# Performance work log

Hardware: AMD Instinct MI355X
Metric: run time of the kernel (lower is better)

The kernel has to match this reference:

```python
import jax, jax.numpy as jnp
import numpy as np

S, H, A = 16384, 1024, 1024


def setup_inputs() -> dict:
    key = jax.random.key(0)
    k1, k2, k3, k4, k5, k6 = jax.random.split(key, 6)
    enc_out = jax.random.normal(k1, (S, 1, H), dtype=jnp.float32)
    dec_h = jax.random.normal(k2, (1, H), dtype=jnp.float32)
    mask = jax.random.randint(k3, (S, 1), 0, 2) == 1  # bool [S,1]
    # learned params (torch Linear stores weight as [out, in]; y = x @ W.T)
    W2_dec = jax.random.normal(k4, (A, H), dtype=jnp.float32) * 0.02
    W1_enc = jax.random.normal(k5, (A, H), dtype=jnp.float32) * 0.02
    V = jax.random.normal(k6, (1, A), dtype=jnp.float32) * 0.02
    return {"enc_out": enc_out, "dec_h": dec_h, "mask": mask,
            "W2_dec": W2_dec, "W1_enc": W1_enc, "V": V}


def reference(enc_out, dec_h, mask, W2_dec, W1_enc, V):
    enc = jnp.squeeze(enc_out, axis=1)            # [S, H]
    d = dec_h @ W2_dec.T                          # [1, A]
    e = enc @ W1_enc.T                            # [S, A]
    u = jnp.tanh(d + e) @ V.T                     # [S, 1]
    u = jnp.where(mask, -jnp.inf, u)              # masked logits (returned, like in-place fill)
    a = jax.nn.softmax(u, axis=0)                 # softmax over seq dim
    out = jnp.sum(a * enc, axis=0)                # [H]
    return (out, u)
```

## Files before the change

kernel.cpp:

```cpp
#include <hip/hip_runtime.h>
#include <math.h>
#include <stdint.h>

#define S_DIM 16384
#define H_DIM 1024
#define A_DIM 1024

#define MASK_NEG (-3.0e38f)

typedef __attribute__((ext_vector_type(8))) _Float16 f16x8;
typedef __attribute__((ext_vector_type(4))) float f32x4;
typedef __attribute__((address_space(3))) uint32_t as3_u32;
typedef __attribute__((address_space(1))) uint32_t as1_u32;

__global__ __launch_bounds__(256) void prep_kernel(
        const float* __restrict__ enc, _Float16* __restrict__ enc_h,
        const float* __restrict__ W1, _Float16* __restrict__ W1_h,
        const float* __restrict__ dec_h, const float* __restrict__ W2,
        float* __restrict__ d, float* __restrict__ u_acc) {
    const int b = blockIdx.x;
    const int t = threadIdx.x;
    if (b < 8704) {
        const float* src = (b < 8192) ? enc : W1;
        _Float16* dst    = (b < 8192) ? enc_h : W1_h;
        const int i = ((b < 8192) ? b : (b - 8192)) * 256 + t;
        float4 v0 = ((const float4*)src)[2 * i];
        float4 v1 = ((const float4*)src)[2 * i + 1];
        union { _Float16 h[8]; uint4 u; } pk;
        pk.h[0] = (_Float16)v0.x; pk.h[1] = (_Float16)v0.y;
        pk.h[2] = (_Float16)v0.z; pk.h[3] = (_Float16)v0.w;
        pk.h[4] = (_Float16)v1.x; pk.h[5] = (_Float16)v1.y;
        pk.h[6] = (_Float16)v1.z; pk.h[7] = (_Float16)v1.w;
        ((uint4*)dst)[i] = pk.u;
        if (b < 64) u_acc[b * 256 + t] = 0.0f;
    } else {
        const int a = b - 8704;
        const float* row = W2 + (size_t)a * H_DIM;
        float s = 0.0f;
        for (int h = t; h < H_DIM; h += 256) s += dec_h[h] * row[h];
        #pragma unroll
        for (int off = 32; off; off >>= 1) s += __shfl_down(s, off, 64);
        __shared__ float wsum[4];
        if ((t & 63) == 0) wsum[t >> 6] = s;
        __syncthreads();
        if (t == 0) d[a] = wsum[0] + wsum[1] + wsum[2] + wsum[3];
    }
}

__global__ __launch_bounds__(512, 2) void fused_gemm_f16(
        const _Float16* __restrict__ Ag,
        const _Float16* __restrict__ Bg,
        const float* __restrict__ V,
        const float* __restrict__ d,
        float* __restrict__ u_acc) {
    __shared__ __align__(16) _Float16 AB[2][16384];

    const int tid  = threadIdx.x;
    const int wave = tid >> 6;
    const int lane = tid & 63;
    const int quad = lane >> 4;
    const int l16  = lane & 15;
    const int wm   = wave >> 2;
    const int wn   = wave & 3;
    const int s0   = blockIdx.x * 256;
    const int a0   = blockIdx.y * 256;

    const _Float16* gsrc = (wave < 4) ? Ag : Bg;
    const int rbase      = (wave < 4) ? s0 : a0;
    const int rowoff     = (wave & 3) * 64;
    const int lrow = lane >> 2;
    const int cg   = ((lane & 3) + (lrow >> 1)) & 3;

    const _Float16* grow[4];
    #pragma unroll
    for (int j = 0; j < 4; ++j)
        grow[j] = gsrc + (size_t)(rbase + rowoff + j * 16 + lrow) * H_DIM + cg * 8;
    _Float16* lbase0 = &AB[0][((wave < 4) ? 0 : 8192) + rowoff * 32];

    const int sw = ((quad - (l16 >> 1)) & 3) * 8;
    int aoff[8], boff[4];
    #pragma unroll
    for (int mi = 0; mi < 8; ++mi)
        aoff[mi] = (wm * 128 + mi * 16 + l16) * 32 + sw;
    #pragma unroll
    for (int ni = 0; ni < 4; ++ni)
        boff[ni] = 8192 + (wn * 64 + ni * 16 + l16) * 32 + sw;

    f32x4 acc[8][4];
    #pragma unroll
    for (int mi = 0; mi < 8; ++mi)
        #pragma unroll
        for (int ni = 0; ni < 4; ++ni)
            acc[mi][ni] = (f32x4){0.f, 0.f, 0.f, 0.f};

    #pragma unroll
    for (int j = 0; j < 4; ++j)
        __builtin_amdgcn_global_load_lds(
            (const as1_u32*)(const void*)(grow[j]),
            (as3_u32*)(void*)(lbase0 + j * 512), 16, 0, 0);
    __syncthreads();

    for (int kt = 0; kt < H_DIM / 32; kt += 2) {
        {
            #pragma unroll
            for (int j = 0; j < 4; ++j)
                __builtin_amdgcn_global_load_lds(
                    (const as1_u32*)(const void*)(grow[j] + (kt + 1) * 32),
                    (as3_u32*)(void*)(lbase0 + 16384 + j * 512), 16, 0, 0);
        }
        {
            f16x8 bf[4];
            #pragma unroll
            for (int ni = 0; ni < 4; ++ni) bf[ni] = *(const f16x8*)&AB[0][boff[ni]];
            #pragma unroll
            for (int mi = 0; mi < 8; ++mi) {
                f16x8 af = *(const f16x8*)&AB[0][aoff[mi]];
                #pragma unroll
                for (int ni = 0; ni < 4; ++ni)
                    acc[mi][ni] = __builtin_amdgcn_mfma_f32_16x16x32_f16(af, bf[ni], acc[mi][ni], 0, 0, 0);
            }
        }
        __syncthreads();

        if (kt + 2 < H_DIM / 32) {
            #pragma unroll
            for (int j = 0; j < 4; ++j)
                __builtin_amdgcn_global_load_lds(
                    (const as1_u32*)(const void*)(grow[j] + (kt + 2) * 32),
                    (as3_u32*)(void*)(lbase0 + j * 512), 16, 0, 0);
        }
        {
            f16x8 bf[4];
            #pragma unroll
            for (int ni = 0; ni < 4; ++ni) bf[ni] = *(const f16x8*)&AB[1][boff[ni]];
            #pragma unroll
            for (int mi = 0; mi < 8; ++mi) {
                f16x8 af = *(const f16x8*)&AB[1][aoff[mi]];
                #pragma unroll
                for (int ni = 0; ni < 4; ++ni)
                    acc[mi][ni] = __builtin_amdgcn_mfma_f32_16x16x32_f16(af, bf[ni], acc[mi][ni], 0, 0, 0);
            }
        }
        __syncthreads();
    }

    float* P = (float*)&AB[0][0];
    float vv[4], dd[4];
    #pragma unroll
    for (int ni = 0; ni < 4; ++ni) {
        int c = a0 + wn * 64 + ni * 16 + l16;
        vv[ni] = V[c];
        dd[ni] = d[c];
    }
    #pragma unroll
    for (int mi = 0; mi < 8; ++mi) {
        #pragma unroll
        for (int reg = 0; reg < 4; ++reg) {
            float s = 0.0f;
            #pragma unroll
            for (int ni = 0; ni < 4; ++ni)
                s += vv[ni] * tanhf(dd[ni] + acc[mi][ni][reg]);
            #pragma unroll
            for (int off = 1; off < 16; off <<= 1)
                s += __shfl_xor(s, off, 64);
            if (l16 == 0)
                P[(wm * 128 + mi * 16 + quad * 4 + reg) * 4 + wn] = s;
        }
    }
    __syncthreads();
    if (tid < 256)
        atomicAdd(u_acc + s0 + tid,
                  P[tid * 4 + 0] + P[tid * 4 + 1] + P[tid * 4 + 2] + P[tid * 4 + 3]);
}

__global__ __launch_bounds__(256) void fused_gemm(const float* __restrict__ enc,
                                                  const float* __restrict__ W1,
                                                  const float* __restrict__ V,
                                                  const float* __restrict__ d,
                                                  float* __restrict__ u_acc) {
    __shared__ __align__(16) float As[16][128 + 4];
    __shared__ __align__(16) float Bs[16][128 + 4];
    const int tid = threadIdx.x;
    const int tx = tid & 15, ty = tid >> 4;
    const int s0 = blockIdx.y * 128, a0 = blockIdx.x * 128;
    const int lr = tid >> 2, lc = tid & 3;
    float acc[8][8] = {};
    for (int kt = 0; kt < H_DIM / 16; ++kt) {
        const int k0 = kt * 16;
        float4 av0 = *(const float4*)(enc + (size_t)(s0 + lr)      * H_DIM + k0 + 4 * lc);
        float4 av1 = *(const float4*)(enc + (size_t)(s0 + lr + 64) * H_DIM + k0 + 4 * lc);
        float4 bv0 = *(const float4*)(W1  + (size_t)(a0 + lr)      * H_DIM + k0 + 4 * lc);
        float4 bv1 = *(const float4*)(W1  + (size_t)(a0 + lr + 64) * H_DIM + k0 + 4 * lc);
        __syncthreads();
        As[4*lc+0][lr] = av0.x; As[4*lc+1][lr] = av0.y; As[4*lc+2][lr] = av0.z; As[4*lc+3][lr] = av0.w;
        As[4*lc+0][lr+64] = av1.x; As[4*lc+1][lr+64] = av1.y; As[4*lc+2][lr+64] = av1.z; As[4*lc+3][lr+64] = av1.w;
        Bs[4*lc+0][lr] = bv0.x; Bs[4*lc+1][lr] = bv0.y; Bs[4*lc+2][lr] = bv0.z; Bs[4*lc+3][lr] = bv0.w;
        Bs[4*lc+0][lr+64] = bv1.x; Bs[4*lc+1][lr+64] = bv1.y; Bs[4*lc+2][lr+64] = bv1.z; Bs[4*lc+3][lr+64] = bv1.w;
        __syncthreads();
        #pragma unroll
        for (int k = 0; k < 16; ++k) {
            float4 A0 = *(const float4*)&As[k][8 * ty];
            float4 A1 = *(const float4*)&As[k][8 * ty + 4];
            float4 B0 = *(const float4*)&Bs[k][8 * tx];
            float4 B1 = *(const float4*)&Bs[k][8 * tx + 4];
            float ar[8] = {A0.x, A0.y, A0.z, A0.w, A1.x, A1.y, A1.z, A1.w};
            float br[8] = {B0.x, B0.y, B0.z, B0.w, B1.x, B1.y, B1.z, B1.w};
            #pragma unroll
            for (int i = 0; i < 8; ++i)
                #pragma unroll
                for (int j = 0; j < 8; ++j)
                    acc[i][j] = fmaf(ar[i], br[j], acc[i][j]);
        }
    }
    float vv[8], dd[8];
    #pragma unroll
    for (int j = 0; j < 8; ++j) { int c = a0 + 8 * tx + j; vv[j] = V[c]; dd[j] = d[c]; }
    float pu[8];
    #pragma unroll
    for (int i = 0; i < 8; ++i) {
        float s = 0.0f;
        #pragma unroll
        for (int j = 0; j < 8; ++j) s += vv[j] * tanhf(dd[j] + acc[i][j]);
        pu[i] = s;
    }
    __syncthreads();
    float* Pf = &As[0][0];
    #pragma unroll
    for (int i = 0; i < 8; ++i) Pf[(8 * ty + i) * 16 + tx] = pu[i];
    __syncthreads();
    if (tid < 128) {
        float s = 0.0f;
        #pragma unroll
        for (int j = 0; j < 16; ++j) s += Pf[tid * 16 + j];
        atomicAdd(u_acc + s0 + tid, s);
    }
}

__global__ __launch_bounds__(1024) void softmax_kernel(const float* __restrict__ u_acc,
                                                       const void* __restrict__ mask,
                                                       float* __restrict__ u_out,
                                                       float* __restrict__ p) {
    const int t = threadIdx.x;
    const unsigned char* mb = (const unsigned char*)mask;
    const int* mi = (const int*)mask;

    unsigned int orv = 0;
    for (int i = t; i < S_DIM; i += 1024)
        if (i & 3) orv |= mb[i];
    __shared__ int sflag;
    if (t == 0) sflag = 0;
    __syncthreads();
    if (orv) sflag = 1;
    __syncthreads();
    const int bytemask = sflag;

    float v[16];
    float lmax = -INFINITY;
    #pragma unroll
    for (int i = 0; i < 16; ++i) {
        int r = t + i * 1024;
        int m = bytemask ? (int)mb[r] : mi[r];
        float val = m ? MASK_NEG : u_acc[r];
        u_out[r] = val;
        v[i] = val;
        lmax = fmaxf(lmax, val);
    }

    __shared__ float red[16];
    __shared__ float sm, sdenom;
    #pragma unroll
    for (int off = 32; off; off >>= 1) lmax = fmaxf(lmax, __shfl_down(lmax, off, 64));
    int wid = t >> 6, lane = t & 63;
    if (lane == 0) red[wid] = lmax;
    __syncthreads();
    if (t == 0) {
        float m2 = -INFINITY;
        for (int i = 0; i < 16; ++i) m2 = fmaxf(m2, red[i]);
        sm = m2;
    }
    __syncthreads();
    const float m = sm;

    float lsum = 0.0f;
    #pragma unroll
    for (int i = 0; i < 16; ++i) {
        v[i] = expf(v[i] - m);
        lsum += v[i];
    }
    #pragma unroll
    for (int off = 32; off; off >>= 1) lsum += __shfl_down(lsum, off, 64);
    if (lane == 0) red[wid] = lsum;
    __syncthreads();
    if (t == 0) {
        float s2 = 0.0f;
        for (int i = 0; i < 16; ++i) s2 += red[i];
        sdenom = s2;
    }
    __syncthreads();
    const float inv = 1.0f / sdenom;
    #pragma unroll
    for (int i = 0; i < 16; ++i) p[t + i * 1024] = v[i] * inv;
}

__global__ __launch_bounds__(256) void wsum_part(const _Float16* __restrict__ enc_h,
                                                 const float* __restrict__ p,
                                                 float* __restrict__ part) {
    const int t = threadIdx.x;
    const int b = blockIdx.x;
    float4 acc = {0.f, 0.f, 0.f, 0.f};
    const int s0 = b * 32;
    for (int s = s0; s < s0 + 32; ++s) {
        float ps = p[s];
        union { _Float16 h[4]; uint2 u; } e;
        e.u = ((const uint2*)(enc_h + (size_t)s * H_DIM))[t];
        acc.x += ps * (float)e.h[0];
        acc.y += ps * (float)e.h[1];
        acc.z += ps * (float)e.h[2];
        acc.w += ps * (float)e.h[3];
    }
    ((float4*)(part + (size_t)b * 1024))[t] = acc;
}
__global__ __launch_bounds__(256) void wsum_reduce(const float* __restrict__ part,
                                                   float* __restrict__ out) {
    __shared__ float red[256];
    const int t = threadIdx.x;
    const int col = blockIdx.x * 16 + (t & 15);
    const int seg = t >> 4;
    float s = 0.0f;
    for (int b = seg * 32; b < seg * 32 + 32; ++b)
        s += part[(size_t)b * 1024 + col];
    red[t] = s;
    __syncthreads();
    if (t < 16) {
        float r = 0.0f;
        #pragma unroll
        for (int k = 0; k < 16; ++k) r += red[k * 16 + t];
        out[col] = r;
    }
}
__global__ __launch_bounds__(256) void weighted_sum(const float* __restrict__ enc,
                                                    const float* __restrict__ p,
                                                    float* __restrict__ out) {
    const int t = threadIdx.x;
    const int s0 = blockIdx.x * 32;
    const float4* encv = (const float4*)enc;
    float4 acc = {0.0f, 0.0f, 0.0f, 0.0f};
    for (int s = s0; s < s0 + 32; ++s) {
        float ps = p[s];
        float4 e = encv[(size_t)s * 256 + t];
        acc.x += ps * e.x; acc.y += ps * e.y; acc.z += ps * e.z; acc.w += ps * e.w;
    }
    atomicAdd(out + 4 * t + 0, acc.x);
    atomicAdd(out + 4 * t + 1, acc.y);
    atomicAdd(out + 4 * t + 2, acc.z);
    atomicAdd(out + 4 * t + 3, acc.w);
}
__global__ void zero_kernel(float* __restrict__ u_acc, float* __restrict__ out) {
    int i = blockIdx.x * 256 + threadIdx.x;
    if (i < S_DIM) u_acc[i] = 0.0f;
    if (i < H_DIM) out[i]   = 0.0f;
}
__global__ __launch_bounds__(256) void dec_proj(const float* __restrict__ dec_h,
                                                const float* __restrict__ W2,
                                                float* __restrict__ d) {
    int a = blockIdx.x;
    int t = threadIdx.x;
    const float* row = W2 + (size_t)a * H_DIM;
    float s = 0.0f;
    for (int h = t; h < H_DIM; h += 256) s += dec_h[h] * row[h];
    #pragma unroll
    for (int off = 32; off; off >>= 1) s += __shfl_down(s, off, 64);
    __shared__ float wsum[4];
    if ((t & 63) == 0) wsum[t >> 6] = s;
    __syncthreads();
    if (t == 0) d[a] = wsum[0] + wsum[1] + wsum[2] + wsum[3];
}

extern "C" void kernel_launch(void* const* d_in, const int* in_sizes, int n_in,
                              void* d_out, int out_size, void* d_ws, size_t ws_size,
                              hipStream_t stream) {
    const float* enc   = (const float*)d_in[0];
    const float* dec_h = (const float*)d_in[1];
    const void*  mask  = d_in[2];
    const float* W2    = (const float*)d_in[3];
    const float* W1    = (const float*)d_in[4];
    const float* V     = (const float*)d_in[5];

    float* out   = (float*)d_out;
    float* u_out = (float*)d_out + H_DIM;

    float* ws    = (float*)d_ws;
    float* d     = ws;
    float* u_acc = ws + A_DIM;
    float* p     = ws + A_DIM + S_DIM;
    float* part  = ws + A_DIM + 2 * S_DIM;
    size_t f_end = (size_t)(A_DIM + 2 * S_DIM + 512 * 1024);
    _Float16* enc_h = (_Float16*)(ws + f_end);
    _Float16* W1_h  = enc_h + (size_t)S_DIM * H_DIM;
    size_t need_bytes = f_end * 4
                      + (size_t)S_DIM * H_DIM * 2
                      + (size_t)A_DIM * H_DIM * 2;

    if (ws_size >= need_bytes) {
        prep_kernel<<<9728, 256, 0, stream>>>(enc, enc_h, W1, W1_h,
                                              dec_h, W2, d, u_acc);
        fused_gemm_f16<<<dim3(S_DIM / 256, A_DIM / 256), 512, 0, stream>>>(
            enc_h, W1_h, V, d, u_acc);
        softmax_kernel<<<1, 1024, 0, stream>>>(u_acc, mask, u_out, p);
        wsum_part<<<S_DIM / 32, 256, 0, stream>>>(enc_h, p, part);
        wsum_reduce<<<64, 256, 0, stream>>>(part, out);
    } else {
        zero_kernel<<<64, 256, 0, stream>>>(u_acc, out);
        dec_proj<<<A_DIM, 256, 0, stream>>>(dec_h, W2, d);
        fused_gemm<<<dim3(A_DIM / 128, S_DIM / 128), 256, 0, stream>>>(enc, W1, V, d, u_acc);
        softmax_kernel<<<1, 1024, 0, stream>>>(u_acc, mask, u_out, p);
        weighted_sum<<<S_DIM / 32, 256, 0, stream>>>(enc, p, out);
    }
}
```

Before: 187.9 us.

## Add deeper-staged fp16 GEMM variant with 64-wide K stages

```diff
diff --git a/kernel.cpp b/kernel.cpp
--- a/kernel.cpp
+++ b/kernel.cpp
@@ -47,13 +47,13 @@
     }
 }
 
-__global__ __launch_bounds__(512, 2) void fused_gemm_f16(
+__global__ __launch_bounds__(512, 1) void fused_gemm_f16_2ph(
         const _Float16* __restrict__ Ag,
         const _Float16* __restrict__ Bg,
         const float* __restrict__ V,
         const float* __restrict__ d,
         float* __restrict__ u_acc) {
-    __shared__ __align__(16) _Float16 AB[2][16384];
+    __shared__ __align__(16) _Float16 AB[2][32768];
 
     const int tid  = threadIdx.x;
     const int wave = tid >> 6;
@@ -93,6 +93,120 @@
         for (int ni = 0; ni < 4; ++ni)
             acc[mi][ni] = (f32x4){0.f, 0.f, 0.f, 0.f};
 
+    const _Float16* hAB = &AB[0][0];
+
+    #pragma unroll
+    for (int s = 0; s < 2; ++s)
+        #pragma unroll
+        for (int j = 0; j < 4; ++j)
+            __builtin_amdgcn_global_load_lds(
+                (const as1_u32*)(const void*)(grow[j] + s * 32),
+                (as3_u32*)(void*)(lbase0 + s * 16384 + j * 512), 16, 0, 0);
+    __syncthreads();
+
+    for (int ph = 0; ph < 16; ++ph) {
+        const int b = ph & 1;
+        if (ph < 15) {
+            #pragma unroll
+            for (int s = 0; s < 2; ++s)
+                #pragma unroll
+                for (int j = 0; j < 4; ++j)
+                    __builtin_amdgcn_global_load_lds(
+                        (const as1_u32*)(const void*)(grow[j] + ((ph + 1) * 2 + s) * 32),
+                        (as3_u32*)(void*)(lbase0 + (b ^ 1) * 32768 + s * 16384 + j * 512),
+                        16, 0, 0);
+        }
+        #pragma unroll
+        for (int s = 0; s < 2; ++s) {
+            const int base = b * 32768 + s * 16384;
+            f16x8 bf[4];
+            #pragma unroll
+            for (int ni = 0; ni < 4; ++ni)
+                bf[ni] = *(const f16x8*)&hAB[base + boff[ni]];
+            #pragma unroll
+            for (int mi = 0; mi < 8; ++mi) {
+                f16x8 af = *(const f16x8*)&hAB[base + aoff[mi]];
+                #pragma unroll
+                for (int ni = 0; ni < 4; ++ni)
+                    acc[mi][ni] = __builtin_amdgcn_mfma_f32_16x16x32_f16(af, bf[ni], acc[mi][ni], 0, 0, 0);
+            }
+        }
+        __syncthreads();
+    }
+
+    float* P = (float*)&AB[0][0];
+    float vv[4], dd[4];
+    #pragma unroll
+    for (int ni = 0; ni < 4; ++ni) {
+        int c = a0 + wn * 64 + ni * 16 + l16;
+        vv[ni] = V[c];
+        dd[ni] = d[c];
+    }
+    #pragma unroll
+    for (int mi = 0; mi < 8; ++mi) {
+        #pragma unroll
+        for (int reg = 0; reg < 4; ++reg) {
+            float s = 0.0f;
+            #pragma unroll
+            for (int ni = 0; ni < 4; ++ni)
+                s += vv[ni] * tanhf(dd[ni] + acc[mi][ni][reg]);
+            #pragma unroll
+            for (int off = 1; off < 16; off <<= 1)
+                s += __shfl_xor(s, off, 64);
+            if (l16 == 0)
+                P[(wm * 128 + mi * 16 + quad * 4 + reg) * 4 + wn] = s;
+        }
+    }
+    __syncthreads();
+    if (tid < 256)
+        atomicAdd(u_acc + s0 + tid,
+                  P[tid * 4 + 0] + P[tid * 4 + 1] + P[tid * 4 + 2] + P[tid * 4 + 3]);
+}
+
+__global__ __launch_bounds__(512, 2) void fused_gemm_f16(
+        const _Float16* __restrict__ Ag, const _Float16* __restrict__ Bg,
+        const float* __restrict__ V, const float* __restrict__ d,
+        float* __restrict__ u_acc) {
+    __shared__ __align__(16) _Float16 AB[2][16384];
+
+    const int tid  = threadIdx.x;
+    const int wave = tid >> 6;
+    const int lane = tid & 63;
+    const int quad = lane >> 4;
+    const int l16  = lane & 15;
+    const int wm   = wave >> 2;
+    const int wn   = wave & 3;
+    const int s0   = blockIdx.x * 256;
+    const int a0   = blockIdx.y * 256;
+
+    const _Float16* gsrc = (wave < 4) ? Ag : Bg;
+    const int rbase      = (wave < 4) ? s0 : a0;
+    const int rowoff     = (wave & 3) * 64;
+    const int lrow = lane >> 2;
+    const int cg   = ((lane & 3) + (lrow >> 1)) & 3;
+
+    const _Float16* grow[4];
+    #pragma unroll
+    for (int j = 0; j < 4; ++j)
+        grow[j] = gsrc + (size_t)(rbase + rowoff + j * 16 + lrow) * H_DIM + cg * 8;
+    _Float16* lbase0 = &AB[0][((wave < 4) ? 0 : 8192) + rowoff * 32];
+
+    const int sw = ((quad - (l16 >> 1)) & 3) * 8;
+    int aoff[8], boff[4];
+    #pragma unroll
+    for (int mi = 0; mi < 8; ++mi)
+        aoff[mi] = (wm * 128 + mi * 16 + l16) * 32 + sw;
+    #pragma unroll
+    for (int ni = 0; ni < 4; ++ni)
+        boff[ni] = 8192 + (wn * 64 + ni * 16 + l16) * 32 + sw;
+
+    f32x4 acc[8][4];
+    #pragma unroll
+    for (int mi = 0; mi < 8; ++mi)
+        #pragma unroll
+        for (int ni = 0; ni < 4; ++ni)
+            acc[mi][ni] = (f32x4){0.f, 0.f, 0.f, 0.f};
+
     #pragma unroll
     for (int j = 0; j < 4; ++j)
         __builtin_amdgcn_global_load_lds(
@@ -121,7 +235,6 @@
             }
         }
         __syncthreads();
-
         if (kt + 2 < H_DIM / 32) {
             #pragma unroll
             for (int j = 0; j < 4; ++j)
@@ -401,11 +514,21 @@
                       + (size_t)S_DIM * H_DIM * 2
                       + (size_t)A_DIM * H_DIM * 2;
 
+    int dev = 0;
+    hipGetDevice(&dev);
+    int max_lds = 0;
+    hipDeviceGetAttribute(&max_lds, hipDeviceAttributeMaxSharedMemoryPerBlock, dev);
+
     if (ws_size >= need_bytes) {
         prep_kernel<<<9728, 256, 0, stream>>>(enc, enc_h, W1, W1_h,
                                               dec_h, W2, d, u_acc);
-        fused_gemm_f16<<<dim3(S_DIM / 256, A_DIM / 256), 512, 0, stream>>>(
-            enc_h, W1_h, V, d, u_acc);
+        if (max_lds >= 131072) {
+            fused_gemm_f16_2ph<<<dim3(S_DIM / 256, A_DIM / 256), 512, 0, stream>>>(
+                enc_h, W1_h, V, d, u_acc);
+        } else {
+            fused_gemm_f16<<<dim3(S_DIM / 256, A_DIM / 256), 512, 0, stream>>>(
+                enc_h, W1_h, V, d, u_acc);
+        }
         softmax_kernel<<<1, 1024, 0, stream>>>(u_acc, mask, u_out, p);
         wsum_part<<<S_DIM / 32, 256, 0, stream>>>(enc_h, p, part);
         wsum_reduce<<<64, 256, 0, stream>>>(part, out);
```

Result: no change. 185.3 us (-1.4%).
